# Kernel tuning notes

Hardware: AMD Instinct MI355X
Metric: run time of the kernel (lower is better)

The kernel has to match this reference:

```python
import jax, jax.numpy as jnp
import numpy as np

HID, OUT, D = 256, 64, 128
N_ITEM, N_USER, E = 100000, 50000, 800000


def sage_conv(x_src, x_dst, src, dst, w_l, b_l, w_r, n_dst):
    # PyG SAGEConv (mean aggr): out = lin_l(mean_j x_src[j]) + lin_r(x_dst)
    msg = x_src[src]                                        # [E, d_src] gather
    agg = jax.ops.segment_sum(msg, dst, num_segments=n_dst)  # [n_dst, d_src]
    cnt = jax.ops.segment_sum(jnp.ones((src.shape[0],), x_src.dtype), dst,
                              num_segments=n_dst)
    mean = agg / jnp.clip(cnt, 1.0, None)[:, None]
    return mean @ w_l + b_l + x_dst @ w_r


def setup_inputs() -> dict:
    key = jax.random.key(0)
    ks = jax.random.split(key, 16)
    sc = lambda d: 1.0 / np.sqrt(d)
    inp = {
        "x_item": jax.random.normal(ks[0], (N_ITEM, D), jnp.float32),
        "x_user": jax.random.normal(ks[1], (N_USER, D), jnp.float32),
        "ei_ii_src": jax.random.randint(ks[2], (E,), 0, N_ITEM),
        "ei_ii_dst": jax.random.randint(ks[3], (E,), 0, N_ITEM),
        "ei_iu_src": jax.random.randint(ks[4], (E,), 0, N_ITEM),
        "ei_iu_dst": jax.random.randint(ks[5], (E,), 0, N_USER),
        # conv1: item->item, in (D, D) -> HID
        "w_l1": jax.random.normal(ks[6], (D, HID), jnp.float32) * sc(D),
        "b1": jnp.zeros((HID,), jnp.float32),
        "w_r1": jax.random.normal(ks[7], (D, HID), jnp.float32) * sc(D),
        # conv2: (item D, user D) -> HID
        "w_l2": jax.random.normal(ks[8], (D, HID), jnp.float32) * sc(D),
        "b2": jnp.zeros((HID,), jnp.float32),
        "w_r2": jax.random.normal(ks[9], (D, HID), jnp.float32) * sc(D),
        # conv3: (item HID, user HID) -> HID
        "w_l3": jax.random.normal(ks[10], (HID, HID), jnp.float32) * sc(HID),
        "b3": jnp.zeros((HID,), jnp.float32),
        "w_r3": jax.random.normal(ks[11], (HID, HID), jnp.float32) * sc(HID),
        # final linear HID -> OUT
        "w_lin": jax.random.normal(ks[12], (HID, OUT), jnp.float32) * sc(HID),
        "b_lin": jnp.zeros((OUT,), jnp.float32),
    }
    return inp


def reference(x_item, x_user, ei_ii_src, ei_ii_dst, ei_iu_src, ei_iu_dst,
              w_l1, b1, w_r1, w_l2, b2, w_r2, w_l3, b3, w_r3, w_lin, b_lin):
    item_x = jax.nn.relu(sage_conv(x_item, x_item, ei_ii_src, ei_ii_dst,
                                   w_l1, b1, w_r1, N_ITEM))
    user_x = jax.nn.relu(sage_conv(x_item, x_user, ei_iu_src, ei_iu_dst,
                                   w_l2, b2, w_r2, N_USER))
    user_x = jax.nn.relu(sage_conv(item_x, user_x, ei_iu_src, ei_iu_dst,
                                   w_l3, b3, w_r3, N_USER))
    return user_x @ w_lin + b_lin
```

## Files before the change

kernel.cpp:

```cpp
#include <hip/hip_runtime.h>
#include <hip/hip_bf16.h>

#define N_ITEM 100000
#define N_USER 50000
#define D_IN   128
#define HID    256
#define OUT_D  64
#define CAP    64

#define S1B   391
#define CV1B  1024
#define CV2B  512
#define PK1B  68
#define G1 (S1B + CV1B + CV2B + PK1B)

#define S2B   391
#define A1B   6250
#define G2 (S2B + A1B)

#define C1B   782
#define A2B   3125
#define G3 (C1B + A2B)

#define C2B   391
#define A3B   3125
#define G4 (C2B + A3B)

typedef __attribute__((ext_vector_type(8))) short bf16x8;
typedef __attribute__((ext_vector_type(4))) float f32x4;

__device__ inline float b2f(unsigned int h) {
    union { unsigned int u; float f; } c; c.u = h << 16; return c.f;
}
__device__ inline unsigned short f2b(float f) {
    unsigned int u = __builtin_bit_cast(unsigned int, f);
    u += 0x7fff + ((u >> 16) & 1);
    return (unsigned short)(u >> 16);
}

__device__ __forceinline__ void scatter_body(
    const int* __restrict__ src, const int* __restrict__ dstl,
    int* __restrict__ cur, int* __restrict__ slot, int E, int t)
{
    int e4 = t * 4;
    if (e4 + 3 < E) {
        int4 d = *(const int4*)&dstl[e4];
        int4 s = *(const int4*)&src[e4];
        int p0 = atomicAdd(&cur[d.x], 1);
        int p1 = atomicAdd(&cur[d.y], 1);
        int p2 = atomicAdd(&cur[d.z], 1);
        int p3 = atomicAdd(&cur[d.w], 1);
        if (p0 < CAP) slot[d.x * CAP + p0] = s.x;
        if (p1 < CAP) slot[d.y * CAP + p1] = s.y;
        if (p2 < CAP) slot[d.z * CAP + p2] = s.z;
        if (p3 < CAP) slot[d.w * CAP + p3] = s.w;
    } else {
        for (int e = e4; e < E; ++e) {
            int d0 = dstl[e], s0 = src[e];
            int p = atomicAdd(&cur[d0], 1);
            if (p < CAP) slot[d0 * CAP + p] = s0;
        }
    }
}

__device__ __forceinline__ void agg_mean128_body(
    const unsigned short* __restrict__ xsrc,
    const int* __restrict__ sl, int num, int hl,
    unsigned short* __restrict__ dstrow)
{
    const unsigned short* xb = xsrc + hl * 4;
    float acc[4] = {};
    int j = 0;
    for (; j + 8 <= num; j += 8) {
        int s[8];
        #pragma unroll
        for (int u = 0; u < 8; ++u) s[u] = sl[j + u];
        uint2 v[8];
        #pragma unroll
        for (int u = 0; u < 8; ++u)
            v[u] = *(const uint2*)(xb + (size_t)s[u] * 256);
        #pragma unroll
        for (int u = 0; u < 8; ++u) {
            acc[0] += b2f(v[u].x & 0xffffu);
            acc[1] += b2f(v[u].x >> 16);
            acc[2] += b2f(v[u].y & 0xffffu);
            acc[3] += b2f(v[u].y >> 16);
        }
    }
    for (; j < num; ++j) {
        uint2 v = *(const uint2*)(xb + (size_t)sl[j] * 256);
        acc[0] += b2f(v.x & 0xffffu);
        acc[1] += b2f(v.x >> 16);
        acc[2] += b2f(v.y & 0xffffu);
        acc[3] += b2f(v.y >> 16);
    }
    float sc = 1.0f / fmaxf((float)num, 1.0f);
    uint2 w;
    w.x = (unsigned int)f2b(acc[0] * sc) | ((unsigned int)f2b(acc[1] * sc) << 16);
    w.y = (unsigned int)f2b(acc[2] * sc) | ((unsigned int)f2b(acc[3] * sc) << 16);
    *(uint2*)(dstrow + hl * 4) = w;
}

__device__ inline void pack_unit(const float* __restrict__ wl,
                                 const float* __restrict__ wr,
                                 int K, int NCv, unsigned short* __restrict__ dst,
                                 int u)
{
    int kb = u / NCv, col = u - kb * NCv;
    int colp = col ^ (kb & 7);
    unsigned short tmp[8];
    #pragma unroll
    for (int j = 0; j < 8; ++j) {
        int k = kb * 8 + j;
        float w = (k < K) ? wl[(size_t)k * NCv + col]
                          : wr[(size_t)(k - K) * NCv + col];
        tmp[j] = f2b(w);
    }
    *(uint4*)&dst[((size_t)kb * NCv + colp) * 8] = *(const uint4*)tmp;
}

__global__ __launch_bounds__(512) void prep1_kernel(
    const int* __restrict__ ii_src, const int* __restrict__ ii_dst,
    int* __restrict__ cur_i, int* __restrict__ slot_ii, int E,
    const float* __restrict__ x_item, const float* __restrict__ x_user,
    unsigned short* __restrict__ Acat1, unsigned short* __restrict__ Acat2,
    const float* __restrict__ wl1, const float* __restrict__ wr1,
    const float* __restrict__ wl2, const float* __restrict__ wr2,
    const float* __restrict__ wl3, const float* __restrict__ wr3,
    const float* __restrict__ wlin,
    unsigned short* __restrict__ Wp1, unsigned short* __restrict__ Wp2,
    unsigned short* __restrict__ Wp3, unsigned short* __restrict__ Wpl)
{
    int b = blockIdx.x;
    if (b < S1B) {
        scatter_body(ii_src, ii_dst, cur_i, slot_ii, E, b * 512 + threadIdx.x);
    } else if (b < S1B + CV1B) {
        const int STR = CV1B * 512;
        for (int u = (b - S1B) * 512 + threadIdx.x; u < N_ITEM * 32; u += STR) {
            int row = u >> 5, c4 = (u & 31) * 4;
            float4 v = *(const float4*)&x_item[(size_t)row * 128 + c4];
            ushort4 o;
            o.x = f2b(v.x); o.y = f2b(v.y); o.z = f2b(v.z); o.w = f2b(v.w);
            *(ushort4*)&Acat1[(size_t)row * 256 + 128 + c4] = o;
        }
    } else if (b < S1B + CV1B + CV2B) {
        const int STR = CV2B * 512;
        for (int u = (b - S1B - CV1B) * 512 + threadIdx.x; u < N_USER * 32; u += STR) {
            int row = u >> 5, c4 = (u & 31) * 4;
            float4 v = *(const float4*)&x_user[(size_t)row * 128 + c4];
            ushort4 o;
            o.x = f2b(v.x); o.y = f2b(v.y); o.z = f2b(v.z); o.w = f2b(v.w);
            *(ushort4*)&Acat2[(size_t)row * 256 + 128 + c4] = o;
        }
    } else {
        int t = (b - S1B - CV1B - CV2B) * 512 + threadIdx.x;
        if (t < 8192)       pack_unit(wl1, wr1, 128, 256, Wp1, t);
        else if (t < 16384) pack_unit(wl2, wr2, 128, 256, Wp2, t - 8192);
        else if (t < 32768) pack_unit(wl3, wr3, 256, 256, Wp3, t - 16384);
        else if (t < 34816) pack_unit(wlin, wlin, 256, 64, Wpl, t - 32768);
    }
}

__global__ __launch_bounds__(512) void prep2_kernel(
    const int* __restrict__ iu_src, const int* __restrict__ iu_dst,
    int* __restrict__ cur_u, int* __restrict__ slot_iu, int E,
    const unsigned short* __restrict__ xsrc,
    const int* __restrict__ slot_ii, const int* __restrict__ cur_i,
    unsigned short* __restrict__ Acat1)
{
    int b = blockIdx.x;
    if (b < S2B) {
        scatter_body(iu_src, iu_dst, cur_u, slot_iu, E, b * 512 + threadIdx.x);
        return;
    }
    int row = (b - S2B) * 16 + (threadIdx.x >> 5);
    int hl = threadIdx.x & 31;
    const int* sl = slot_ii + (size_t)row * CAP;
    int num = min(cur_i[row], CAP);
    agg_mean128_body(xsrc, sl, num, hl, Acat1 + (size_t)row * 256);
}

template <int NC, int WM, int WN, bool OUT_BF16, bool RELU>
__device__ __forceinline__ void gemm_body(
    int bid,
    const unsigned short* __restrict__ A, int lda,
    const unsigned short* __restrict__ Wp,
    const float* __restrict__ bias,
    void* __restrict__ Cout, int ldc, int col_off,
    int nrows, int nkt)
{
    constexpr int BM = 128;
    constexpr int MR = WM / 16, NR = WN / 16;
    constexpr int NWC = NC / WN;
    __shared__ unsigned short As[BM * 64];
    __shared__ unsigned short Bs[64 * NC];

    const int tid  = threadIdx.x;
    const int wave = tid >> 6;
    const int lane = tid & 63;
    const int row0 = bid * BM;
    const int wr = wave / NWC;
    const int wc = wave % NWC;

    f32x4 acc[MR][NR];
    #pragma unroll
    for (int m = 0; m < MR; ++m)
        #pragma unroll
        for (int n = 0; n < NR; ++n)
            acc[m][n] = (f32x4){0.f, 0.f, 0.f, 0.f};

    for (int kt = 0; kt < nkt; ++kt) {
        #pragma unroll
        for (int c = 0; c < 2; ++c) {
            int i = wave * 2 + c;
            int rl = 8 * i + (lane >> 3);
            int kc = (lane & 7) ^ (lane >> 3);
            const unsigned short* g =
                A + (size_t)(row0 + rl) * lda + kt * 64 + kc * 8;
            __builtin_amdgcn_global_load_lds(
                (const __attribute__((address_space(1))) void*)g,
                (__attribute__((address_space(3))) void*)(As + i * 512), 16, 0, 0);
        }
        constexpr int BCALLS = (64 * NC * 2) / 1024;
        constexpr int PW = BCALLS / 8;
        #pragma unroll
        for (int c = 0; c < PW; ++c) {
            int j = wave * PW + c;
            const unsigned short* g =
                Wp + (size_t)kt * (8 * NC * 8) + (size_t)j * 512 + lane * 8;
            __builtin_amdgcn_global_load_lds(
                (const __attribute__((address_space(1))) void*)g,
                (__attribute__((address_space(3))) void*)(Bs + j * 512), 16, 0, 0);
        }
        __syncthreads();

        #pragma unroll
        for (int kk = 0; kk < 2; ++kk) {
            bf16x8 af[MR], bfr[NR];
            #pragma unroll
            for (int m = 0; m < MR; ++m) {
                int row = wr * WM + m * 16 + (lane & 15);
                int kc = ((kk * 4) + (lane >> 4)) ^ (lane & 7);
                af[m] = *(const bf16x8*)(As + row * 64 + kc * 8);
            }
            #pragma unroll
            for (int n = 0; n < NR; ++n) {
                int kb = kk * 4 + (lane >> 4);
                int col = (wc * WN + n * 16 + (lane & 15)) ^ (kb & 7);
                bfr[n] = *(const bf16x8*)(Bs + (kb * NC + col) * 8);
            }
            #pragma unroll
            for (int m = 0; m < MR; ++m)
                #pragma unroll
                for (int n = 0; n < NR; ++n)
                    acc[m][n] = __builtin_amdgcn_mfma_f32_16x16x32_bf16(
                        af[m], bfr[n], acc[m][n], 0, 0, 0);
        }
        __syncthreads();
    }

    #pragma unroll
    for (int n = 0; n < NR; ++n) {
        int col = wc * WN + n * 16 + (lane & 15);
        float bv = bias[col];
        #pragma unroll
        for (int m = 0; m < MR; ++m) {
            #pragma unroll
            for (int j = 0; j < 4; ++j) {
                int row = row0 + wr * WM + m * 16 + (lane >> 4) * 4 + j;
                if (row < nrows) {
                    float v = acc[m][n][j] + bv;
                    if (RELU) v = fmaxf(v, 0.f);
                    if (OUT_BF16)
                        ((unsigned short*)Cout)[(size_t)row * ldc + col_off + col] = f2b(v);
                    else
                        ((float*)Cout)[(size_t)row * ldc + col_off + col] = v;
                }
            }
        }
    }
}

template <int NC, int WM, int WN, bool OUT_BF16, bool RELU>
__global__ __launch_bounds__(512) void gemm_mfma(
    const unsigned short* __restrict__ A, int lda,
    const unsigned short* __restrict__ Wp,
    const float* __restrict__ bias,
    void* __restrict__ Cout, int ldc, int col_off,
    int nrows, int nkt)
{
    gemm_body<NC, WM, WN, OUT_BF16, RELU>(blockIdx.x, A, lda, Wp, bias,
                                          Cout, ldc, col_off, nrows, nkt);
}

__global__ __launch_bounds__(512) void conv1_agg2_kernel(
    const unsigned short* __restrict__ Acat1,
    const unsigned short* __restrict__ Wp1,
    const float* __restrict__ b1,
    unsigned short* __restrict__ item_x,
    const unsigned short* __restrict__ xsrc,
    const int* __restrict__ slot_iu, const int* __restrict__ cur_u,
    unsigned short* __restrict__ Acat2)
{
    if (blockIdx.x < C1B) {
        gemm_body<256, 64, 64, true, true>(blockIdx.x, Acat1, 256, Wp1, b1,
                                           item_x, 256, 0, N_ITEM, 4);
        return;
    }
    int b = blockIdx.x - C1B;
    int row = b * 16 + (threadIdx.x >> 5);
    int hl = threadIdx.x & 31;
    const int* sl = slot_iu + (size_t)row * CAP;
    int num = min(cur_u[row], CAP);
    agg_mean128_body(xsrc, sl, num, hl, Acat2 + (size_t)row * 256);
}

__global__ __launch_bounds__(512) void conv2_agg3_kernel(
    const unsigned short* __restrict__ Acat2,
    const unsigned short* __restrict__ Wp2,
    const float* __restrict__ b2,
    unsigned short* __restrict__ Acat3,
    const unsigned short* __restrict__ item_x,
    const int* __restrict__ slot_iu, const int* __restrict__ cur_u)
{
    if (blockIdx.x < C2B) {
        gemm_body<256, 64, 64, true, true>(blockIdx.x, Acat2, 256, Wp2, b2,
                                           Acat3, 512, 256, N_USER, 4);
        return;
    }
    int b = blockIdx.x - C2B;
    int row = b * 16 + (threadIdx.x >> 5);
    int hl = threadIdx.x & 31;
    const int* sl = slot_iu + (size_t)row * CAP;
    int num = min(cur_u[row], CAP);
    const unsigned short* xb = item_x + hl * 8;
    float acc[8] = {};

    int j = 0;
    for (; j + 8 <= num; j += 8) {
        int s[8];
        #pragma unroll
        for (int u = 0; u < 8; ++u) s[u] = sl[j + u];
        uint4 v[8];
        #pragma unroll
        for (int u = 0; u < 8; ++u)
            v[u] = *(const uint4*)(xb + (size_t)s[u] * 256);
        #pragma unroll
        for (int u = 0; u < 8; ++u) {
            acc[0] += b2f(v[u].x & 0xffffu);
            acc[1] += b2f(v[u].x >> 16);
            acc[2] += b2f(v[u].y & 0xffffu);
            acc[3] += b2f(v[u].y >> 16);
            acc[4] += b2f(v[u].z & 0xffffu);
            acc[5] += b2f(v[u].z >> 16);
            acc[6] += b2f(v[u].w & 0xffffu);
            acc[7] += b2f(v[u].w >> 16);
        }
    }
    for (; j < num; ++j) {
        uint4 v = *(const uint4*)(xb + (size_t)sl[j] * 256);
        acc[0] += b2f(v.x & 0xffffu);
        acc[1] += b2f(v.x >> 16);
        acc[2] += b2f(v.y & 0xffffu);
        acc[3] += b2f(v.y >> 16);
        acc[4] += b2f(v.z & 0xffffu);
        acc[5] += b2f(v.z >> 16);
        acc[6] += b2f(v.w & 0xffffu);
        acc[7] += b2f(v.w >> 16);
    }

    float sc = 1.0f / fmaxf((float)num, 1.0f);
    uint4 w;
    w.x = (unsigned int)f2b(acc[0] * sc) | ((unsigned int)f2b(acc[1] * sc) << 16);
    w.y = (unsigned int)f2b(acc[2] * sc) | ((unsigned int)f2b(acc[3] * sc) << 16);
    w.z = (unsigned int)f2b(acc[4] * sc) | ((unsigned int)f2b(acc[5] * sc) << 16);
    w.w = (unsigned int)f2b(acc[6] * sc) | ((unsigned int)f2b(acc[7] * sc) << 16);
    *(uint4*)(Acat3 + (size_t)row * 512 + hl * 8) = w;
}

extern "C" void kernel_launch(void* const* d_in, const int* in_sizes, int n_in,
                              void* d_out, int out_size, void* d_ws, size_t ws_size,
                              hipStream_t stream)
{
    const float* x_item = (const float*)d_in[0];
    const float* x_user = (const float*)d_in[1];
    const int* ii_src   = (const int*)d_in[2];
    const int* ii_dst   = (const int*)d_in[3];
    const int* iu_src   = (const int*)d_in[4];
    const int* iu_dst   = (const int*)d_in[5];
    const float* w_l1 = (const float*)d_in[6];
    const float* b1   = (const float*)d_in[7];
    const float* w_r1 = (const float*)d_in[8];
    const float* w_l2 = (const float*)d_in[9];
    const float* b2   = (const float*)d_in[10];
    const float* w_r2 = (const float*)d_in[11];
    const float* w_l3 = (const float*)d_in[12];
    const float* b3   = (const float*)d_in[13];
    const float* w_r3 = (const float*)d_in[14];
    const float* w_lin = (const float*)d_in[15];
    const float* b_lin = (const float*)d_in[16];
    float* out = (float*)d_out;

    const int E = in_sizes[2];
    const int NIP = 100096;
    const int NUP = 50048;

    int* cur_i   = (int*)d_ws;
    int* cur_u   = cur_i + 100352;
    int* slot_ii = cur_u + 50176;
    int* slot_iu = slot_ii + (size_t)N_ITEM * CAP;

    unsigned short* Acat1  = (unsigned short*)(slot_iu + (size_t)N_USER * CAP);
    unsigned short* item_x = Acat1  + (size_t)NIP * 256;
    unsigned short* Acat2  = item_x + (size_t)NIP * 256;
    unsigned short* Acat3  = Acat2  + (size_t)NUP * 256;
    unsigned short* ux3    = Acat3  + (size_t)NUP * 512;
    unsigned short* Wp1    = ux3    + (size_t)NUP * 256;
    unsigned short* Wp2    = Wp1 + 65536;
    unsigned short* Wp3    = Wp2 + 65536;
    unsigned short* Wpl    = Wp3 + 131072;

    hipMemsetAsync(cur_i, 0, (size_t)150528 * 4, stream);

    prep1_kernel<<<G1, 512, 0, stream>>>(
        ii_src, ii_dst, cur_i, slot_ii, E,
        x_item, x_user, Acat1, Acat2,
        w_l1, w_r1, w_l2, w_r2, w_l3, w_r3, w_lin,
        Wp1, Wp2, Wp3, Wpl);

    prep2_kernel<<<G2, 512, 0, stream>>>(
        iu_src, iu_dst, cur_u, slot_iu, E,
        Acat1 + 128, slot_ii, cur_i, Acat1);

    conv1_agg2_kernel<<<G3, 512, 0, stream>>>(
        Acat1, Wp1, b1, item_x,
        Acat1 + 128, slot_iu, cur_u, Acat2);

    conv2_agg3_kernel<<<G4, 512, 0, stream>>>(
        Acat2, Wp2, b2, Acat3, item_x, slot_iu, cur_u);

    gemm_mfma<256, 64, 64, true, true><<<NUP / 128, 512, 0, stream>>>(
        Acat3, 512, Wp3, b3, ux3, 256, 0, N_USER, 8);

    gemm_mfma<64, 16, 64, false, false><<<NUP / 128, 512, 0, stream>>>(
        ux3, 256, Wpl, b_lin, out, 64, 0, N_USER, 4);
}
```

Baseline: 359.5 us.

## Split conv3 aggregation and GEMMs into halves to overlap stages

Widens the 128-dim mean aggregation to 16 lanes per row with 16-byte loads, so each block covers 32 rows and the agg grids are halved. It also splits the conv3 aggregation into a low and a high half of user rows. The conv3 GEMM and the final linear on the low half are co-scheduled in the same launches as the remaining aggregation and GEMM of the high half. This aims to hide tail latency and fill the GPU across stages, at the cost of extra launches and row-range bookkeeping that must match between kernels.

```diff
diff --git a/kernel.cpp b/kernel.cpp
--- a/kernel.cpp
+++ b/kernel.cpp
@@ -15,16 +15,26 @@
 #define G1 (S1B + CV1B + CV2B + PK1B)
 
 #define S2B   391
-#define A1B   6250
+#define A1B   3125
 #define G2 (S2B + A1B)
 
 #define C1B   782
-#define A2B   3125
+#define A2B   1563
 #define G3 (C1B + A2B)
 
 #define C2B   391
-#define A3B   3125
-#define G4 (C2B + A3B)
+#define A3LB  1568
+#define G4 (C2B + A3LB)
+
+#define C3LB  196
+#define A3HB  1557
+#define G5 (C3LB + A3HB)
+
+#define C3HB  195
+#define FLB   196
+#define G6 (C3HB + FLB)
+
+#define FHB   195
 
 typedef __attribute__((ext_vector_type(8))) short bf16x8;
 typedef __attribute__((ext_vector_type(4))) float f32x4;
@@ -63,42 +73,100 @@
     }
 }
 
-__device__ __forceinline__ void agg_mean128_body(
+__device__ __forceinline__ void agg_mean128_q(
     const unsigned short* __restrict__ xsrc,
-    const int* __restrict__ sl, int num, int hl,
+    const int* __restrict__ sl, int num, int ql,
     unsigned short* __restrict__ dstrow)
 {
-    const unsigned short* xb = xsrc + hl * 4;
-    float acc[4] = {};
+    const unsigned short* xb = xsrc + ql * 8;
+    float acc[8] = {};
     int j = 0;
     for (; j + 8 <= num; j += 8) {
         int s[8];
         #pragma unroll
         for (int u = 0; u < 8; ++u) s[u] = sl[j + u];
-        uint2 v[8];
+        uint4 v[8];
         #pragma unroll
         for (int u = 0; u < 8; ++u)
-            v[u] = *(const uint2*)(xb + (size_t)s[u] * 256);
+            v[u] = *(const uint4*)(xb + (size_t)s[u] * 256);
         #pragma unroll
         for (int u = 0; u < 8; ++u) {
             acc[0] += b2f(v[u].x & 0xffffu);
             acc[1] += b2f(v[u].x >> 16);
             acc[2] += b2f(v[u].y & 0xffffu);
             acc[3] += b2f(v[u].y >> 16);
+            acc[4] += b2f(v[u].z & 0xffffu);
+            acc[5] += b2f(v[u].z >> 16);
+            acc[6] += b2f(v[u].w & 0xffffu);
+            acc[7] += b2f(v[u].w >> 16);
         }
     }
     for (; j < num; ++j) {
-        uint2 v = *(const uint2*)(xb + (size_t)sl[j] * 256);
+        uint4 v = *(const uint4*)(xb + (size_t)sl[j] * 256);
         acc[0] += b2f(v.x & 0xffffu);
         acc[1] += b2f(v.x >> 16);
         acc[2] += b2f(v.y & 0xffffu);
         acc[3] += b2f(v.y >> 16);
+        acc[4] += b2f(v.z & 0xffffu);
+        acc[5] += b2f(v.z >> 16);
+        acc[6] += b2f(v.w & 0xffffu);
+        acc[7] += b2f(v.w >> 16);
     }
     float sc = 1.0f / fmaxf((float)num, 1.0f);
-    uint2 w;
+    uint4 w;
     w.x = (unsigned int)f2b(acc[0] * sc) | ((unsigned int)f2b(acc[1] * sc) << 16);
     w.y = (unsigned int)f2b(acc[2] * sc) | ((unsigned int)f2b(acc[3] * sc) << 16);
-    *(uint2*)(dstrow + hl * 4) = w;
+    w.z = (unsigned int)f2b(acc[4] * sc) | ((unsigned int)f2b(acc[5] * sc) << 16);
+    w.w = (unsigned int)f2b(acc[6] * sc) | ((unsigned int)f2b(acc[7] * sc) << 16);
+    *(uint4*)(dstrow + ql * 8) = w;
+}
+
+__device__ __forceinline__ void agg_mean256_body(
+    const unsigned short* __restrict__ xsrc,
+    const int* __restrict__ sl, int num, int hl,
+    unsigned short* __restrict__ dstrow)
+{
+    const unsigned short* xb = xsrc + hl * 8;
+    float acc[8] = {};
+    int j = 0;
+    for (; j + 8 <= num; j += 8) {
+        int s[8];
+        #pragma unroll
+        for (int u = 0; u < 8; ++u) s[u] = sl[j + u];
+        uint4 v[8];
+        #pragma unroll
+        for (int u = 0; u < 8; ++u)
+            v[u] = *(const uint4*)(xb + (size_t)s[u] * 256);
+        #pragma unroll
+        for (int u = 0; u < 8; ++u) {
+            acc[0] += b2f(v[u].x & 0xffffu);
+            acc[1] += b2f(v[u].x >> 16);
+            acc[2] += b2f(v[u].y & 0xffffu);
+            acc[3] += b2f(v[u].y >> 16);
+            acc[4] += b2f(v[u].z & 0xffffu);
+            acc[5] += b2f(v[u].z >> 16);
+            acc[6] += b2f(v[u].w & 0xffffu);
+            acc[7] += b2f(v[u].w >> 16);
+        }
+    }
+    for (; j < num; ++j) {
+        uint4 v = *(const uint4*)(xb + (size_t)sl[j] * 256);
+        acc[0] += b2f(v.x & 0xffffu);
+        acc[1] += b2f(v.x >> 16);
+        acc[2] += b2f(v.y & 0xffffu);
+        acc[3] += b2f(v.y >> 16);
+        acc[4] += b2f(v.z & 0xffffu);
+        acc[5] += b2f(v.z >> 16);
+        acc[6] += b2f(v.w & 0xffffu);
+        acc[7] += b2f(v.w >> 16);
+    }
+    float sc = 1.0f / fmaxf((float)num, 1.0f);
+    uint4 w;
+    w.x = (unsigned int)f2b(acc[0] * sc) | ((unsigned int)f2b(acc[1] * sc) << 16);
+    w.y = (unsigned int)f2b(acc[2] * sc) | ((unsigned int)f2b(acc[3] * sc) << 16);
+    w.z = (unsigned int)f2b(acc[4] * sc) | ((unsigned int)f2b(acc[5] * sc) << 16);
+    w.w = (unsigned int)f2b(acc[6] * sc) | ((unsigned int)f2b(acc[7] * sc) << 16);
+    *(uint4*)(dstrow + hl * 8) = w;
 }
 
 __device__ inline void pack_unit(const float* __restrict__ wl,
@@ -173,11 +241,11 @@
         scatter_body(iu_src, iu_dst, cur_u, slot_iu, E, b * 512 + threadIdx.x);
         return;
     }
-    int row = (b - S2B) * 16 + (threadIdx.x >> 5);
-    int hl = threadIdx.x & 31;
+    int row = (b - S2B) * 32 + (threadIdx.x >> 4);
+    int ql = threadIdx.x & 15;
     const int* sl = slot_ii + (size_t)row * CAP;
     int num = min(cur_i[row], CAP);
-    agg_mean128_body(xsrc, sl, num, hl, Acat1 + (size_t)row * 256);
+    agg_mean128_q(xsrc, sl, num, ql, Acat1 + (size_t)row * 256);
 }
 
 template <int NC, int WM, int WN, bool OUT_BF16, bool RELU>
@@ -283,14 +351,15 @@
 
 template <int NC, int WM, int WN, bool OUT_BF16, bool RELU>
 __global__ __launch_bounds__(512) void gemm_mfma(
+    int bid_base,
     const unsigned short* __restrict__ A, int lda,
     const unsigned short* __restrict__ Wp,
     const float* __restrict__ bias,
     void* __restrict__ Cout, int ldc, int col_off,
     int nrows, int nkt)
 {
-    gemm_body<NC, WM, WN, OUT_BF16, RELU>(blockIdx.x, A, lda, Wp, bias,
-                                          Cout, ldc, col_off, nrows, nkt);
+    gemm_body<NC, WM, WN, OUT_BF16, RELU>(bid_base + blockIdx.x, A, lda, Wp,
+                                          bias, Cout, ldc, col_off, nrows, nkt);
 }
 
 __global__ __launch_bounds__(512) void conv1_agg2_kernel(
@@ -307,12 +376,12 @@
                                            item_x, 256, 0, N_ITEM, 4);
         return;
     }
-    int b = blockIdx.x - C1B;
-    int row = b * 16 + (threadIdx.x >> 5);
-    int hl = threadIdx.x & 31;
+    int row = (blockIdx.x - C1B) * 32 + (threadIdx.x >> 4);
+    if (row >= N_USER) return;
+    int ql = threadIdx.x & 15;
     const int* sl = slot_iu + (size_t)row * CAP;
     int num = min(cur_u[row], CAP);
-    agg_mean128_body(xsrc, sl, num, hl, Acat2 + (size_t)row * 256);
+    agg_mean128_q(xsrc, sl, num, ql, Acat2 + (size_t)row * 256);
 }
 
 __global__ __launch_bounds__(512) void conv2_agg3_kernel(
@@ -328,54 +397,50 @@
                                            Acat3, 512, 256, N_USER, 4);
         return;
     }
-    int b = blockIdx.x - C2B;
-    int row = b * 16 + (threadIdx.x >> 5);
+    int row = (blockIdx.x - C2B) * 16 + (threadIdx.x >> 5);
     int hl = threadIdx.x & 31;
     const int* sl = slot_iu + (size_t)row * CAP;
     int num = min(cur_u[row], CAP);
-    const unsigned short* xb = item_x + hl * 8;
-    float acc[8] = {};
-
-    int j = 0;
-    for (; j + 8 <= num; j += 8) {
-        int s[8];
-        #pragma unroll
-        for (int u = 0; u < 8; ++u) s[u] = sl[j + u];
-        uint4 v[8];
-        #pragma unroll
-        for (int u = 0; u < 8; ++u)
-            v[u] = *(const uint4*)(xb + (size_t)s[u] * 256);
-        #pragma unroll
-        for (int u = 0; u < 8; ++u) {
-            acc[0] += b2f(v[u].x & 0xffffu);
-            acc[1] += b2f(v[u].x >> 16);
-            acc[2] += b2f(v[u].y & 0xffffu);
-            acc[3] += b2f(v[u].y >> 16);
-            acc[4] += b2f(v[u].z & 0xffffu);
-            acc[5] += b2f(v[u].z >> 16);
-            acc[6] += b2f(v[u].w & 0xffffu);
-            acc[7] += b2f(v[u].w >> 16);
-        }
-    }
-    for (; j < num; ++j) {
-        uint4 v = *(const uint4*)(xb + (size_t)sl[j] * 256);
-        acc[0] += b2f(v.x & 0xffffu);
-        acc[1] += b2f(v.x >> 16);
-        acc[2] += b2f(v.y & 0xffffu);
-        acc[3] += b2f(v.y >> 16);
-        acc[4] += b2f(v.z & 0xffffu);
-        acc[5] += b2f(v.z >> 16);
-        acc[6] += b2f(v.w & 0xffffu);
-        acc[7] += b2f(v.w >> 16);
-    }
-
-    float sc = 1.0f / fmaxf((float)num, 1.0f);
-    uint4 w;
-    w.x = (unsigned int)f2b(acc[0] * sc) | ((unsigned int)f2b(acc[1] * sc) << 16);
-    w.y = (unsigned int)f2b(acc[2] * sc) | ((unsigned int)f2b(acc[3] * sc) << 16);
-    w.z = (unsigned int)f2b(acc[4] * sc) | ((unsigned int)f2b(acc[5] * sc) << 16);
-    w.w = (unsigned int)f2b(acc[6] * sc) | ((unsigned int)f2b(acc[7] * sc) << 16);
-    *(uint4*)(Acat3 + (size_t)row * 512 + hl * 8) = w;
+    agg_mean256_body(item_x, sl, num, hl, Acat3 + (size_t)row * 512);
+}
+
+__global__ __launch_bounds__(512) void conv3_agg3b_kernel(
+    const unsigned short* __restrict__ Acat3r,
+    unsigned short* __restrict__ Acat3w,
+    const unsigned short* __restrict__ Wp3,
+    const float* __restrict__ b3,
+    unsigned short* __restrict__ ux3,
+    const unsigned short* __restrict__ item_x,
+    const int* __restrict__ slot_iu, const int* __restrict__ cur_u)
+{
+    if (blockIdx.x < C3LB) {
+        gemm_body<256, 64, 64, true, true>(blockIdx.x, Acat3r, 512, Wp3, b3,
+                                           ux3, 256, 0, N_USER, 8);
+        return;
+    }
+    int row = 25088 + (blockIdx.x - C3LB) * 16 + (threadIdx.x >> 5);
+    int hl = threadIdx.x & 31;
+    const int* sl = slot_iu + (size_t)row * CAP;
+    int num = min(cur_u[row], CAP);
+    agg_mean256_body(item_x, sl, num, hl, Acat3w + (size_t)row * 512);
+}
+
+__global__ __launch_bounds__(512) void conv3b_final_kernel(
+    const unsigned short* __restrict__ Acat3,
+    const unsigned short* __restrict__ Wp3,
+    const float* __restrict__ b3,
+    unsigned short* __restrict__ ux3,
+    const unsigned short* __restrict__ Wpl,
+    const float* __restrict__ b_lin,
+    float* __restrict__ out)
+{
+    if (blockIdx.x < C3HB) {
+        gemm_body<256, 64, 64, true, true>(C3LB + blockIdx.x, Acat3, 512, Wp3,
+                                           b3, ux3, 256, 0, N_USER, 8);
+    } else {
+        gemm_body<64, 16, 64, false, false>(blockIdx.x - C3HB, ux3, 256, Wpl,
+                                            b_lin, out, 64, 0, N_USER, 4);
+    }
 }
 
 extern "C" void kernel_launch(void* const* d_in, const int* in_sizes, int n_in,
@@ -439,9 +504,12 @@
     conv2_agg3_kernel<<<G4, 512, 0, stream>>>(
         Acat2, Wp2, b2, Acat3, item_x, slot_iu, cur_u);
 
-    gemm_mfma<256, 64, 64, true, true><<<NUP / 128, 512, 0, stream>>>(
-        Acat3, 512, Wp3, b3, ux3, 256, 0, N_USER, 8);
-
-    gemm_mfma<64, 16, 64, false, false><<<NUP / 128, 512, 0, stream>>>(
-        ux3, 256, Wpl, b_lin, out, 64, 0, N_USER, 4);
-}
+    conv3_agg3b_kernel<<<G5, 512, 0, stream>>>(
+        Acat3, Acat3, Wp3, b3, ux3, item_x, slot_iu, cur_u);
+
+    conv3b_final_kernel<<<G6, 512, 0, stream>>>(
+        Acat3, Wp3, b3, ux3, Wpl, b_lin, out);
+
+    gemm_mfma<64, 16, 64, false, false><<<FHB, 512, 0, stream>>>(
+        FLB, ux3, 256, Wpl, b_lin, out, 64, 0, N_USER, 4);
+}
```

Measured after the change: 370.2 us. 1.03x slower.
